# Optimization experiments

Hardware: AMD Instinct MI355X
Metric: run time of the kernel (lower is better)

Reference implementation:

```python
import jax, jax.numpy as jnp
import numpy as np

B, T, C = 2, 2048, 1024
NH = 16
HS = C // NH

def setup_inputs() -> dict:
    key = jax.random.key(0)
    ks = jax.random.split(key, 5)
    x = jax.random.normal(ks[0], (B, T, C), dtype=jnp.float32)
    scale = 1.0 / np.sqrt(C)
    Wk = jax.random.normal(ks[1], (C, C), dtype=jnp.float32) * scale
    bk = jax.random.normal(ks[2], (C,), dtype=jnp.float32) * scale
    Wv = jax.random.normal(ks[3], (C, C), dtype=jnp.float32) * scale
    bv = jax.random.normal(ks[4], (C,), dtype=jnp.float32) * scale
    return {"x": x, "Wk": Wk, "bk": bk, "Wv": Wv, "bv": bv}

def reference(x, Wk, bk, Wv, bv):
    b, t, c = x.shape
    # projections: key and value are Dense; query is identity (as in source)
    k = (x @ Wk + bk).reshape(b, t, NH, HS).transpose(0, 2, 1, 3)  # b nh T hs
    q = x.reshape(b, t, NH, HS).transpose(0, 2, 1, 3)              # b nh T hs
    v = (x @ Wv + bv).reshape(b, t, NH, HS).transpose(0, 2, 1, 3)  # b nh T hs
    # NOTE: source computes logits = K @ Q^T (no 1/sqrt(d) scaling)
    logits = jnp.einsum('bhid,bhjd->bhij', k, q)                   # b nh T T
    causal = jnp.tril(jnp.ones((t, t), dtype=bool))                # True where allowed
    masked = jnp.where(causal[None, None, :, :], logits, -jnp.inf)
    att = jax.nn.softmax(masked, axis=-1)
    y = jnp.einsum('bhij,bhjd->bhid', att, v)                      # b nh T hs
    return y.transpose(0, 2, 1, 3).reshape(b, t, c)
```

## Files before the change

### kernel.cpp

```cpp
#include <hip/hip_runtime.h>
#include <cstdint>
#include <cstddef>

#define BB  2
#define TT  2048
#define CC  1024
#define NHH 16
#define HSS 64
#define BT  (BB*TT)

typedef unsigned short u16;
typedef unsigned int u32;
typedef _Float16 f16;
typedef __attribute__((ext_vector_type(8))) _Float16 f16x8;
typedef __attribute__((ext_vector_type(8))) __bf16 bf16x8;
typedef __attribute__((ext_vector_type(4))) float f32x4;

__device__ __forceinline__ u16 f2bf(float f) {
    union { float f; u32 u; } x; x.f = f;
    return (u16)((x.u + 0x7fffu + ((x.u >> 16) & 1u)) >> 16);
}
__device__ __forceinline__ u16 f2h(float f) {
    union { f16 h; u16 u; } x; x.h = (f16)f;
    return x.u;
}

#define MFMA_BF(a,b,c) __builtin_amdgcn_mfma_f32_16x16x32_bf16((a),(b),(c),0,0,0)
#define MFMA_F16(a,b,c) __builtin_amdgcn_mfma_f32_16x16x32_f16((a),(b),(c),0,0,0)

__device__ __forceinline__ void gld16(const u16* g, u16* l) {
    __builtin_amdgcn_global_load_lds(
        (const __attribute__((address_space(1))) unsigned int*)g,
        (__attribute__((address_space(3))) unsigned int*)l, 16, 0, 0);
}

__global__ __launch_bounds__(256) void convert_x(
    const float* __restrict__ X, u16* __restrict__ Xf)
{
    const int idx = (blockIdx.x * 256 + threadIdx.x) * 8;
    const float4 a = *(const float4*)&X[idx];
    const float4 b = *(const float4*)&X[idx + 4];
    float v[8] = {a.x, a.y, a.z, a.w, b.x, b.y, b.z, b.w};
    union { uint4 u; u16 s[8]; } H;
    #pragma unroll
    for (int u = 0; u < 8; ++u) H.s[u] = f2h(v[u]);
    *(uint4*)&Xf[idx] = H.u;
}

__global__ __launch_bounds__(256) void convert_w(
    const float* __restrict__ Wk, const float* __restrict__ Wv,
    u16* __restrict__ WkT, u16* __restrict__ WvT)
{
    const bool isK = (blockIdx.z == 0);
    const float* W = isK ? Wk : Wv;
    u16* WT = isK ? WkT : WvT;
    __shared__ __align__(16) u16 LH[64][72];
    const int tid = threadIdx.x;
    const int k0 = blockIdx.y * 64, n0 = blockIdx.x * 64;
    {
        const int row = tid >> 2, coff = (tid & 3) * 16;
        const float* g = &W[(size_t)(k0 + row) * CC + n0 + coff];
        #pragma unroll
        for (int u = 0; u < 16; ++u) LH[row][coff + u] = f2h(g[u]);
    }
    __syncthreads();
    {
        const int n = tid >> 2, kc = (tid & 3) * 16;
        union { uint4 u[2]; u16 s[16]; } Hq;
        #pragma unroll
        for (int u = 0; u < 16; ++u) Hq.s[u] = LH[kc + u][n];
        uint4* ph = (uint4*)&WT[(size_t)(n0 + n) * CC + k0 + kc];
        ph[0] = Hq.u[0]; ph[1] = Hq.u[1];
    }
}

__global__ __launch_bounds__(256) void proj_kernel(
    const u16* __restrict__ Xf, const u16* __restrict__ WkT,
    const u16* __restrict__ WvT,
    const float* __restrict__ bk, const float* __restrict__ bv,
    u16* __restrict__ Kf, u16* __restrict__ Vt)
{
    __shared__ u16 SM[4][8192];

    const int id = blockIdx.x;
    const int xcd = id & 7, idx = id >> 3;
    const int z = idx >> 5, rem = idx & 31;
    const int n0 = (rem & 7) * 128;
    const int m0 = (xcd * 4 + (rem >> 3)) * 128;
    const bool isK = (z == 0);
    const u16* WT = isK ? WkT : WvT;

    const int tid = threadIdx.x;
    const int w = tid >> 6, lane = tid & 63;
    const int quad = lane >> 4, l15 = lane & 15;
    const int wm = (w >> 1) * 64, wn = (w & 1) * 64;

    const u16* src = (w < 2) ? Xf : WT;
    const int rb = (w < 2) ? m0 : n0;
    int srow[8], scg[8];
    #pragma unroll
    for (int t = 0; t < 8; ++t) {
        int ci = (w & 1) * 512 + t * 64 + lane;
        srow[t] = ci >> 3;
        scg[t] = ((ci & 7) - srow[t]) & 7;
    }
    const int sbase = (w & 1) * 4096;

    f32x4 acc[4][4] = {};

    {
        u16* dst = ((w < 2) ? SM[0] : SM[2]) + sbase;
        #pragma unroll
        for (int t = 0; t < 8; ++t)
            gld16(src + (size_t)(rb + srow[t]) * CC + scg[t] * 8, dst + t * 512);
    }

    for (int ki = 0; ki < 16; ++ki) {
        const int buf = ki & 1;
        __syncthreads();
        if (ki < 15) {
            u16* dst = ((w < 2) ? SM[buf ^ 1] : SM[2 + (buf ^ 1)]) + sbase;
            const int k0n = (ki + 1) * 64;
            #pragma unroll
            for (int t = 0; t < 8; ++t)
                gld16(src + (size_t)(rb + srow[t]) * CC + k0n + scg[t] * 8,
                      dst + t * 512);
        }
        const u16* Ab = SM[buf];
        const u16* Bb = SM[2 + buf];
        #pragma unroll
        for (int kk = 0; kk < 2; ++kk) {
            f16x8 ah[4];
            #pragma unroll
            for (int i = 0; i < 4; ++i) {
                const int row = wm + i * 16 + l15;
                const int cp = ((kk * 4 + quad + row) & 7) * 8;
                ah[i] = *(const f16x8*)&Ab[row * 64 + cp];
            }
            #pragma unroll
            for (int j = 0; j < 4; ++j) {
                const int rowb = wn + j * 16 + l15;
                const int cpb = ((kk * 4 + quad + rowb) & 7) * 8;
                f16x8 bh_ = *(const f16x8*)&Bb[rowb * 64 + cpb];
                #pragma unroll
                for (int i = 0; i < 4; ++i)
                    acc[i][j] = MFMA_F16(ah[i], bh_, acc[i][j]);
            }
        }
    }

    __syncthreads();
    u16* XL = &SM[0][0];

    if (isK) {
        #pragma unroll
        for (int j = 0; j < 4; ++j) {
            const float bias = bk[n0 + wn + j * 16 + l15];
            #pragma unroll
            for (int i = 0; i < 4; ++i)
                #pragma unroll
                for (int r = 0; r < 4; ++r)
                    XL[(wm + i * 16 + quad * 4 + r) * 136 + wn + j * 16 + l15] =
                        f2h(acc[i][j][r] + bias);
        }
        __syncthreads();
        const int r = tid >> 1, half = tid & 1;
        #pragma unroll
        for (int t = 0; t < 8; ++t)
            *(uint4*)&Kf[(size_t)(m0 + r) * CC + n0 + half * 64 + t * 8] =
                *(const uint4*)&XL[r * 136 + half * 64 + t * 8];
    } else {
        #pragma unroll
        for (int j = 0; j < 4; ++j) {
            const float bias = bv[n0 + wn + j * 16 + l15];
            #pragma unroll
            for (int i = 0; i < 4; ++i) {
                uint2 pk;
                pk.x = (u32)f2bf(acc[i][j][0] + bias) |
                       ((u32)f2bf(acc[i][j][1] + bias) << 16);
                pk.y = (u32)f2bf(acc[i][j][2] + bias) |
                       ((u32)f2bf(acc[i][j][3] + bias) << 16);
                *(uint2*)&XL[(wn + j * 16 + l15) * 136 + wm + i * 16 + quad * 4] = pk;
            }
        }
        __syncthreads();
        const int nl = tid >> 1, half = tid & 1;
        const int d = (n0 + nl) & (HSS - 1), hh = (n0 + nl) >> 6;
        const int bb = m0 >> 11, tb = (m0 & (TT - 1)) + half * 64;
        const size_t gb = ((size_t)(bb * NHH + hh) * HSS + d) * TT + tb;
        #pragma unroll
        for (int t = 0; t < 8; ++t)
            *(uint4*)&Vt[gb + t * 8] = *(const uint4*)&XL[nl * 136 + half * 64 + t * 8];
    }
}

__global__ __launch_bounds__(256) void attn_kernel(
    const u16* __restrict__ Xf, const u16* __restrict__ Kf,
    const u16* __restrict__ Vt, float* __restrict__ out)
{
    __shared__ u16 Xs[2][4096];
    __shared__ u16 Vs[2][4096];
    __shared__ __align__(16) u16 Ps[4][2][1152];

    const int L = blockIdx.x;
    const int xcd = L & 7, k = (L >> 3) & 15, grp = L >> 7;
    const int hb = xcd + 8 * grp;
    const int h = hb & (NHH - 1), b = hb >> 4;
    const int iA = k, iB = 31 - k;
    const int i0A = iA * 64, i0B = iB * 64;

    const int tid = threadIdx.x;
    const int w = tid >> 6, lane = tid & 63;
    const int quad = lane >> 4, l15 = lane & 15;
    const size_t rowbase = (size_t)b * TT;
    const int hd = h * HSS;
    const size_t vgbase = (size_t)(b * NHH + h) * HSS * TT;

    bf16x8 ones;
    { union { u32 u[4]; bf16x8 v; } o;
      #pragma unroll
      for (int i = 0; i < 4; ++i) o.u[i] = 0x3F803F80u;
      ones = o.v; }

    f16x8 qA[2], qB[2];
    #pragma unroll
    for (int c = 0; c < 2; ++c) {
        qA[c] = *(const f16x8*)&Kf[(rowbase + i0A + w * 16 + l15) * CC + hd + c * 32 + quad * 8];
        qB[c] = *(const f16x8*)&Kf[(rowbase + i0B + w * 16 + l15) * CC + hd + c * 32 + quad * 8];
    }

    int crow[2], ccg[2], cbase[2];
    #pragma unroll
    for (int t = 0; t < 2; ++t) {
        const int ci = t * 256 + tid;
        crow[t] = ci >> 3;
        ccg[t] = ((ci & 7) - crow[t]) & 7;
        cbase[t] = (t * 256 + w * 64) * 8;
    }
    const u16* gx[2]; const u16* gv[2];
    #pragma unroll
    for (int t = 0; t < 2; ++t) {
        gx[t] = Xf + (rowbase + crow[t]) * CC + hd + ccg[t] * 8;
        gv[t] = Vt + vgbase + (size_t)crow[t] * TT + ccg[t] * 8;
    }

    #pragma unroll
    for (int t = 0; t < 2; ++t) {
        gld16(gx[t], Xs[0] + cbase[t]);
        gld16(gv[t], Vs[0] + cbase[t]);
    }

    f32x4 oA[4] = {}, oB[4] = {};
    f32x4 laA = {}, laB = {};

    for (int jt = 0; jt <= iB; ++jt) {
        const int buf = jt & 1;
        __syncthreads();
        if (jt < iB) {
            const int j0n = (jt + 1) * 64;
            #pragma unroll
            for (int t = 0; t < 2; ++t) {
                gld16(gx[t] + (size_t)j0n * CC, Xs[buf ^ 1] + cbase[t]);
                gld16(gv[t] + j0n, Vs[buf ^ 1] + cbase[t]);
            }
        }
        const bool doA = (jt <= iA);

        f32x4 sB[4], sA[4];
        #pragma unroll
        for (int nt = 0; nt < 4; ++nt) {
            const int krow = nt * 16 + l15;
            f16x8 x0 = *(const f16x8*)&Xs[buf][krow * 64 + ((quad + krow) & 7) * 8];
            f16x8 x1 = *(const f16x8*)&Xs[buf][krow * 64 + ((quad + 4 + krow) & 7) * 8];
            f32x4 z = {};
            z = MFMA_F16(qB[0], x0, z);
            z = MFMA_F16(qB[1], x1, z);
            sB[nt] = z;
            if (doA) {
                f32x4 y = {};
                y = MFMA_F16(qA[0], x0, y);
                y = MFMA_F16(qA[1], x1, y);
                sA[nt] = y;
            }
        }
        if (jt == iB) {
            #pragma unroll
            for (int nt = 0; nt < 4; ++nt) {
                const int jg = nt * 16 + l15;
                #pragma unroll
                for (int r = 0; r < 4; ++r)
                    if (jg > w * 16 + quad * 4 + r) sB[nt][r] = -1e30f;
            }
        }
        if (doA && jt == iA) {
            #pragma unroll
            for (int nt = 0; nt < 4; ++nt) {
                const int jg = nt * 16 + l15;
                #pragma unroll
                for (int r = 0; r < 4; ++r)
                    if (jg > w * 16 + quad * 4 + r) sA[nt][r] = -1e30f;
            }
        }

        #pragma unroll
        for (int nt = 0; nt < 4; ++nt)
            #pragma unroll
            for (int r = 0; r < 4; ++r)
                Ps[w][0][(quad * 4 + r) * 72 + nt * 16 + l15] =
                    f2bf(__expf(sB[nt][r] - 20.f));
        if (doA) {
            #pragma unroll
            for (int nt = 0; nt < 4; ++nt)
                #pragma unroll
                for (int r = 0; r < 4; ++r)
                    Ps[w][1][(quad * 4 + r) * 72 + nt * 16 + l15] =
                        f2bf(__expf(sA[nt][r] - 20.f));
        }

        bf16x8 aB0 = *(const bf16x8*)&Ps[w][0][l15 * 72 + quad * 8];
        bf16x8 aB1 = *(const bf16x8*)&Ps[w][0][l15 * 72 + 32 + quad * 8];
        laB = MFMA_BF(aB0, ones, laB);
        laB = MFMA_BF(aB1, ones, laB);
        bf16x8 aA0, aA1;
        if (doA) {
            aA0 = *(const bf16x8*)&Ps[w][1][l15 * 72 + quad * 8];
            aA1 = *(const bf16x8*)&Ps[w][1][l15 * 72 + 32 + quad * 8];
            laA = MFMA_BF(aA0, ones, laA);
            laA = MFMA_BF(aA1, ones, laA);
        }

        #pragma unroll
        for (int dt = 0; dt < 4; ++dt) {
            const int vrow = dt * 16 + l15;
            bf16x8 v0 = *(const bf16x8*)&Vs[buf][vrow * 64 + ((quad + vrow) & 7) * 8];
            bf16x8 v1 = *(const bf16x8*)&Vs[buf][vrow * 64 + ((quad + 4 + vrow) & 7) * 8];
            oB[dt] = MFMA_BF(aB0, v0, oB[dt]);
            oB[dt] = MFMA_BF(aB1, v1, oB[dt]);
            if (doA) {
                oA[dt] = MFMA_BF(aA0, v0, oA[dt]);
                oA[dt] = MFMA_BF(aA1, v1, oA[dt]);
            }
        }
    }

    float liA[4], liB[4];
    #pragma unroll
    for (int r = 0; r < 4; ++r) { liA[r] = 1.f / laA[r]; liB[r] = 1.f / laB[r]; }
    #pragma unroll
    for (int dt = 0; dt < 4; ++dt) {
        #pragma unroll
        for (int r = 0; r < 4; ++r) {
            const int igA = i0A + w * 16 + quad * 4 + r;
            const int igB = i0B + w * 16 + quad * 4 + r;
            out[(rowbase + igA) * CC + hd + dt * 16 + l15] = oA[dt][r] * liA[r];
            out[(rowbase + igB) * CC + hd + dt * 16 + l15] = oB[dt][r] * liB[r];
        }
    }
}

extern "C" void kernel_launch(void* const* d_in, const int* in_sizes, int n_in,
                              void* d_out, int out_size, void* d_ws, size_t ws_size,
                              hipStream_t stream) {
    (void)in_sizes; (void)n_in; (void)out_size; (void)ws_size;
    const float* x  = (const float*)d_in[0];
    const float* Wk = (const float*)d_in[1];
    const float* bk = (const float*)d_in[2];
    const float* Wv = (const float*)d_in[3];
    const float* bv = (const float*)d_in[4];
    float* out = (float*)d_out;

    const size_t M4 = (size_t)BT * CC;
    const size_t M1 = (size_t)CC * CC;
    u16* Xf  = (u16*)d_ws;
    u16* Kf  = Xf + M4;
    u16* Vt  = Kf + M4;
    u16* WkT = Vt + M4;
    u16* WvT = WkT + M1;

    convert_x<<<dim3(M4 / (256 * 8)), 256, 0, stream>>>(x, Xf);
    convert_w<<<dim3(16, 16, 2), 256, 0, stream>>>(Wk, Wv, WkT, WvT);
    proj_kernel<<<dim3(512), 256, 0, stream>>>(Xf, WkT, WvT, bk, bv, Kf, Vt);
    attn_kernel<<<dim3(512), 256, 0, stream>>>(Xf, Kf, Vt, out);
}
```

Measured before the change: 154.2 us.

## Assign one causal query tile per wave, halving attention blocks

The attention kernel is reorganised so that each of the four waves in a block owns a full 64-row query tile (k, 15-k, 16+k, 31-k), rather than each block splitting two tiles across its waves. The grid shrinks from 512 to 256 blocks, and the shared X/V tiles now feed four query tiles per load. The row-sum is now accumulated with VALU adds plus a shuffle reduction instead of an MFMA against ones. Each wave holds more accumulator registers and waves within a block have unbalanced amounts of work, which may hurt occupancy and lead to idle waves.

```diff
diff --git a/kernel.cpp b/kernel.cpp
--- a/kernel.cpp
+++ b/kernel.cpp
@@ -198,44 +198,35 @@
     const u16* __restrict__ Xf, const u16* __restrict__ Kf,
     const u16* __restrict__ Vt, float* __restrict__ out)
 {
-    __shared__ u16 Xs[2][4096];
-    __shared__ u16 Vs[2][4096];
-    __shared__ __align__(16) u16 Ps[4][2][1152];
+    __shared__ __align__(16) u16 Xs[2][4096];
+    __shared__ __align__(16) u16 Vs[2][4096];
+    __shared__ __align__(16) u16 Ps[4][64 * 72];
+    __shared__ float lbuf[4][64];
 
     const int L = blockIdx.x;
-    const int xcd = L & 7, k = (L >> 3) & 15, grp = L >> 7;
-    const int hb = xcd + 8 * grp;
+    const int xcd = L & 7, k = (L >> 3) & 7, g = L >> 6;
+    const int hb = xcd + 8 * g;
     const int h = hb & (NHH - 1), b = hb >> 4;
-    const int iA = k, iB = 31 - k;
-    const int i0A = iA * 64, i0B = iB * 64;
 
     const int tid = threadIdx.x;
     const int w = tid >> 6, lane = tid & 63;
     const int quad = lane >> 4, l15 = lane & 15;
+
+    const int itw = (w == 0) ? k : (w == 1) ? 15 - k : (w == 2) ? 16 + k : 31 - k;
+    const int i0w = itw * 64;
+    const int jmax = 31 - k;
+
     const size_t rowbase = (size_t)b * TT;
     const int hd = h * HSS;
     const size_t vgbase = (size_t)(b * NHH + h) * HSS * TT;
 
-    bf16x8 ones;
-    { union { u32 u[4]; bf16x8 v; } o;
-      #pragma unroll
-      for (int i = 0; i < 4; ++i) o.u[i] = 0x3F803F80u;
-      ones = o.v; }
-
-    f16x8 qA[2], qB[2];
-    #pragma unroll
-    for (int c = 0; c < 2; ++c) {
-        qA[c] = *(const f16x8*)&Kf[(rowbase + i0A + w * 16 + l15) * CC + hd + c * 32 + quad * 8];
-        qB[c] = *(const f16x8*)&Kf[(rowbase + i0B + w * 16 + l15) * CC + hd + c * 32 + quad * 8];
-    }
-
-    int crow[2], ccg[2], cbase[2];
+    int crow[2], ccg[2], cb[2];
     #pragma unroll
     for (int t = 0; t < 2; ++t) {
         const int ci = t * 256 + tid;
         crow[t] = ci >> 3;
         ccg[t] = ((ci & 7) - crow[t]) & 7;
-        cbase[t] = (t * 256 + w * 64) * 8;
+        cb[t] = (t * 256 + w * 64) * 8;
     }
     const u16* gx[2]; const u16* gv[2];
     #pragma unroll
@@ -244,117 +235,101 @@
         gv[t] = Vt + vgbase + (size_t)crow[t] * TT + ccg[t] * 8;
     }
 
+    f16x8 qf[4][2];
+    #pragma unroll
+    for (int s = 0; s < 4; ++s)
+        #pragma unroll
+        for (int c = 0; c < 2; ++c)
+            qf[s][c] = *(const f16x8*)&Kf[(rowbase + i0w + s * 16 + l15) * CC
+                                          + hd + c * 32 + quad * 8];
+
     #pragma unroll
     for (int t = 0; t < 2; ++t) {
-        gld16(gx[t], Xs[0] + cbase[t]);
-        gld16(gv[t], Vs[0] + cbase[t]);
-    }
-
-    f32x4 oA[4] = {}, oB[4] = {};
-    f32x4 laA = {}, laB = {};
-
-    for (int jt = 0; jt <= iB; ++jt) {
+        gld16(gx[t], Xs[0] + cb[t]);
+        gld16(gv[t], Vs[0] + cb[t]);
+    }
+
+    f32x4 o[4][4] = {};
+    float lsum[4] = {0.f, 0.f, 0.f, 0.f};
+
+    for (int jt = 0; jt <= jmax; ++jt) {
         const int buf = jt & 1;
         __syncthreads();
-        if (jt < iB) {
-            const int j0n = (jt + 1) * 64;
+        if (jt < jmax) {
+            const size_t j0n = (size_t)(jt + 1) * 64;
             #pragma unroll
             for (int t = 0; t < 2; ++t) {
-                gld16(gx[t] + (size_t)j0n * CC, Xs[buf ^ 1] + cbase[t]);
-                gld16(gv[t] + j0n, Vs[buf ^ 1] + cbase[t]);
-            }
-        }
-        const bool doA = (jt <= iA);
-
-        f32x4 sB[4], sA[4];
-        #pragma unroll
-        for (int nt = 0; nt < 4; ++nt) {
-            const int krow = nt * 16 + l15;
-            f16x8 x0 = *(const f16x8*)&Xs[buf][krow * 64 + ((quad + krow) & 7) * 8];
-            f16x8 x1 = *(const f16x8*)&Xs[buf][krow * 64 + ((quad + 4 + krow) & 7) * 8];
-            f32x4 z = {};
-            z = MFMA_F16(qB[0], x0, z);
-            z = MFMA_F16(qB[1], x1, z);
-            sB[nt] = z;
-            if (doA) {
-                f32x4 y = {};
-                y = MFMA_F16(qA[0], x0, y);
-                y = MFMA_F16(qA[1], x1, y);
-                sA[nt] = y;
-            }
-        }
-        if (jt == iB) {
-            #pragma unroll
-            for (int nt = 0; nt < 4; ++nt) {
-                const int jg = nt * 16 + l15;
+                gld16(gx[t] + j0n * CC, Xs[buf ^ 1] + cb[t]);
+                gld16(gv[t] + j0n, Vs[buf ^ 1] + cb[t]);
+            }
+        }
+        if (jt <= itw) {
+            const bool diag = (jt == itw);
+            #pragma unroll
+            for (int jg = 0; jg < 4; ++jg) {
+                const int jrow = jg * 16 + l15;
+                f16x8 a0 = *(const f16x8*)&Xs[buf][jrow * 64 + ((quad + jrow) & 7) * 8];
+                f16x8 a1 = *(const f16x8*)&Xs[buf][jrow * 64 + ((quad + 4 + jrow) & 7) * 8];
                 #pragma unroll
-                for (int r = 0; r < 4; ++r)
-                    if (jg > w * 16 + quad * 4 + r) sB[nt][r] = -1e30f;
-            }
-        }
-        if (doA && jt == iA) {
-            #pragma unroll
-            for (int nt = 0; nt < 4; ++nt) {
-                const int jg = nt * 16 + l15;
+                for (int s = 0; s < 4; ++s) {
+                    f32x4 z = {};
+                    z = MFMA_F16(a0, qf[s][0], z);
+                    z = MFMA_F16(a1, qf[s][1], z);
+                    if (diag) {
+                        #pragma unroll
+                        for (int r = 0; r < 4; ++r)
+                            if (jg * 16 + quad * 4 + r > s * 16 + l15) z[r] = -1e30f;
+                    }
+                    const float e0 = __expf(z[0] - 20.f);
+                    const float e1 = __expf(z[1] - 20.f);
+                    const float e2 = __expf(z[2] - 20.f);
+                    const float e3 = __expf(z[3] - 20.f);
+                    lsum[s] += (e0 + e1) + (e2 + e3);
+                    uint2 pk;
+                    pk.x = (u32)f2bf(e0) | ((u32)f2bf(e1) << 16);
+                    pk.y = (u32)f2bf(e2) | ((u32)f2bf(e3) << 16);
+                    *(uint2*)&Ps[w][(s * 16 + l15) * 72 + jg * 16 + quad * 4] = pk;
+                }
+            }
+            bf16x8 vf[4][2];
+            #pragma unroll
+            for (int dt = 0; dt < 4; ++dt) {
+                const int vrow = dt * 16 + l15;
+                vf[dt][0] = *(const bf16x8*)&Vs[buf][vrow * 64 + ((quad + vrow) & 7) * 8];
+                vf[dt][1] = *(const bf16x8*)&Vs[buf][vrow * 64 + ((quad + 4 + vrow) & 7) * 8];
+            }
+            #pragma unroll
+            for (int s = 0; s < 4; ++s) {
+                bf16x8 ap0 = *(const bf16x8*)&Ps[w][(s * 16 + l15) * 72 + quad * 8];
+                bf16x8 ap1 = *(const bf16x8*)&Ps[w][(s * 16 + l15) * 72 + 32 + quad * 8];
                 #pragma unroll
-                for (int r = 0; r < 4; ++r)
-                    if (jg > w * 16 + quad * 4 + r) sA[nt][r] = -1e30f;
-            }
-        }
-
-        #pragma unroll
-        for (int nt = 0; nt < 4; ++nt)
+                for (int dt = 0; dt < 4; ++dt) {
+                    o[s][dt] = MFMA_BF(ap0, vf[dt][0], o[s][dt]);
+                    o[s][dt] = MFMA_BF(ap1, vf[dt][1], o[s][dt]);
+                }
+            }
+        }
+    }
+
+    #pragma unroll
+    for (int s = 0; s < 4; ++s) {
+        float v = lsum[s];
+        v += __shfl_xor(v, 16, 64);
+        v += __shfl_xor(v, 32, 64);
+        if (quad == 0) lbuf[w][s * 16 + l15] = v;
+    }
+    #pragma unroll
+    for (int s = 0; s < 4; ++s) {
+        const f32x4 lv = *(const f32x4*)&lbuf[w][s * 16 + quad * 4];
+        f32x4 li;
+        #pragma unroll
+        for (int r = 0; r < 4; ++r) li[r] = 1.f / lv[r];
+        const int igb = i0w + s * 16 + quad * 4;
+        #pragma unroll
+        for (int dt = 0; dt < 4; ++dt)
             #pragma unroll
             for (int r = 0; r < 4; ++r)
-                Ps[w][0][(quad * 4 + r) * 72 + nt * 16 + l15] =
-                    f2bf(__expf(sB[nt][r] - 20.f));
-        if (doA) {
-            #pragma unroll
-            for (int nt = 0; nt < 4; ++nt)
-                #pragma unroll
-                for (int r = 0; r < 4; ++r)
-                    Ps[w][1][(quad * 4 + r) * 72 + nt * 16 + l15] =
-                        f2bf(__expf(sA[nt][r] - 20.f));
-        }
-
-        bf16x8 aB0 = *(const bf16x8*)&Ps[w][0][l15 * 72 + quad * 8];
-        bf16x8 aB1 = *(const bf16x8*)&Ps[w][0][l15 * 72 + 32 + quad * 8];
-        laB = MFMA_BF(aB0, ones, laB);
-        laB = MFMA_BF(aB1, ones, laB);
-        bf16x8 aA0, aA1;
-        if (doA) {
-            aA0 = *(const bf16x8*)&Ps[w][1][l15 * 72 + quad * 8];
-            aA1 = *(const bf16x8*)&Ps[w][1][l15 * 72 + 32 + quad * 8];
-            laA = MFMA_BF(aA0, ones, laA);
-            laA = MFMA_BF(aA1, ones, laA);
-        }
-
-        #pragma unroll
-        for (int dt = 0; dt < 4; ++dt) {
-            const int vrow = dt * 16 + l15;
-            bf16x8 v0 = *(const bf16x8*)&Vs[buf][vrow * 64 + ((quad + vrow) & 7) * 8];
-            bf16x8 v1 = *(const bf16x8*)&Vs[buf][vrow * 64 + ((quad + 4 + vrow) & 7) * 8];
-            oB[dt] = MFMA_BF(aB0, v0, oB[dt]);
-            oB[dt] = MFMA_BF(aB1, v1, oB[dt]);
-            if (doA) {
-                oA[dt] = MFMA_BF(aA0, v0, oA[dt]);
-                oA[dt] = MFMA_BF(aA1, v1, oA[dt]);
-            }
-        }
-    }
-
-    float liA[4], liB[4];
-    #pragma unroll
-    for (int r = 0; r < 4; ++r) { liA[r] = 1.f / laA[r]; liB[r] = 1.f / laB[r]; }
-    #pragma unroll
-    for (int dt = 0; dt < 4; ++dt) {
-        #pragma unroll
-        for (int r = 0; r < 4; ++r) {
-            const int igA = i0A + w * 16 + quad * 4 + r;
-            const int igB = i0B + w * 16 + quad * 4 + r;
-            out[(rowbase + igA) * CC + hd + dt * 16 + l15] = oA[dt][r] * liA[r];
-            out[(rowbase + igB) * CC + hd + dt * 16 + l15] = oB[dt][r] * liB[r];
-        }
+                out[(rowbase + igb + r) * CC + hd + dt * 16 + l15] = o[s][dt][r] * li[r];
     }
 }
 
@@ -380,5 +355,5 @@
     convert_x<<<dim3(M4 / (256 * 8)), 256, 0, stream>>>(x, Xf);
     convert_w<<<dim3(16, 16, 2), 256, 0, stream>>>(Wk, Wv, WkT, WvT);
     proj_kernel<<<dim3(512), 256, 0, stream>>>(Xf, WkT, WvT, bk, bv, Kf, Vt);
-    attn_kernel<<<dim3(512), 256, 0, stream>>>(Xf, Kf, Vt, out);
-}
+    attn_kernel<<<dim3(256), 256, 0, stream>>>(Xf, Kf, Vt, out);
+}
```

Result: slower. 182.2 us (+18.1%).
